# Performance work log

Hardware: AMD Instinct MI355X
Metric: run time of the kernel (lower is better)

The kernel has to match this reference:

```python
import jax, jax.numpy as jnp
from jax import lax
import numpy as np

B, CIN, COUT, D, TDIM, E = 2, 16, 8, 96, 256, 8


def setup_inputs() -> dict:
    key = jax.random.key(0)
    ks = jax.random.split(key, 12)
    s = lambda fan: 1.0 / np.sqrt(fan)
    return {
        "x": jax.random.normal(ks[0], (B, CIN, D, D, D), jnp.float32),
        "text_features": jax.random.normal(ks[1], (B, TDIM), jnp.float32),
        # expert weight basis [E, Cout, Cin, 3, 3, 3] (kaiming-uniform-ish)
        "weight_basis": jax.random.uniform(ks[2], (E, COUT, CIN, 3, 3, 3), jnp.float32, -s(CIN * 27), s(CIN * 27)),
        "bias_basis": jnp.zeros((E, COUT), jnp.float32),
        # router MLP: text_dim -> 64 -> E
        "r_w1": jax.random.uniform(ks[3], (TDIM, 64), jnp.float32, -s(TDIM), s(TDIM)),
        "r_b1": jax.random.uniform(ks[4], (64,), jnp.float32, -s(TDIM), s(TDIM)),
        "r_w2": jax.random.uniform(ks[5], (64, E), jnp.float32, -s(64), s(64)),
        "r_b2": jax.random.uniform(ks[6], (E,), jnp.float32, -s(64), s(64)),
        # modulator MLP: text_dim -> 64 -> Cout
        "m_w1": jax.random.uniform(ks[7], (TDIM, 64), jnp.float32, -s(TDIM), s(TDIM)),
        "m_b1": jax.random.uniform(ks[8], (64,), jnp.float32, -s(TDIM), s(TDIM)),
        "m_w2": jax.random.uniform(ks[9], (64, COUT), jnp.float32, -s(64), s(64)),
        "m_b2": jax.random.uniform(ks[10], (COUT,), jnp.float32, -s(64), s(64)),
    }


def reference(x, text_features, weight_basis, bias_basis,
              r_w1, r_b1, r_w2, r_b2, m_w1, m_b1, m_w2, m_b2):
    b, cin = x.shape[0], x.shape[1]
    cout = weight_basis.shape[1]
    # router -> softmax routing weights over experts
    h = jax.nn.leaky_relu(text_features @ r_w1 + r_b1, 0.1)
    router_logits = h @ r_w2 + r_b2                      # [b, E]
    routing_weights = jax.nn.softmax(router_logits, -1)  # [b, E]
    # modulator -> per-sample channel gates
    g = jax.nn.leaky_relu(text_features @ m_w1 + m_b1, 0.1)
    gamma = jax.nn.sigmoid(g @ m_w2 + m_b2)              # [b, Cout]
    # per-sample dynamic conv weights via expert mixing
    cw = jnp.einsum('be,eoixyz->boixyz', routing_weights, weight_basis)  # [b,Cout,Cin,3,3,3]
    cb = routing_weights @ bias_basis                                    # [b, Cout]
    # grouped-conv trick: batch folded into channels, groups=b
    xr = x.reshape(1, b * cin, *x.shape[2:])
    wr = cw.reshape(b * cout, cin, 3, 3, 3)
    out = lax.conv_general_dilated(
        xr, wr, window_strides=(1, 1, 1), padding=[(1, 1)] * 3,
        dimension_numbers=('NCDHW', 'OIDHW', 'NCDHW'), feature_group_count=b)
    out = out.reshape(b, cout, *out.shape[2:]) + cb[:, :, None, None, None]
    out = out * (1.0 + gamma[:, :, None, None, None])
    return out, router_logits, routing_weights
```

## Files before the change

### kernel.cpp

```cpp
#include <hip/hip_runtime.h>
#include <math.h>

#define NB 2
#define CIN 16
#define COUT 8
#define DD 96
#define TDIM 256
#define NE 8
#define VOX (DD*DD*DD)
#define OUT_ELEMS (NB*COUT*VOX)

#define XT_BYTES ((size_t)NB * VOX * 32)
#define WS_A_F 7168
#define WS_D_F 7184

#define LX 18
#define PLANE (LX*LX)
#define NVX (PLANE*5)
#define HALFB (NVX*16)

typedef _Float16 f16x8 __attribute__((ext_vector_type(8)));
typedef _Float16 f16x4 __attribute__((ext_vector_type(4)));
typedef float f32x4 __attribute__((ext_vector_type(4)));

__global__ void setup_kernel(const float* __restrict__ text,
                             const float* __restrict__ wb,
                             const float* __restrict__ bb,
                             const float* __restrict__ rw1, const float* __restrict__ rb1,
                             const float* __restrict__ rw2, const float* __restrict__ rb2,
                             const float* __restrict__ mw1, const float* __restrict__ mb1,
                             const float* __restrict__ mw2, const float* __restrict__ mb2,
                             float* __restrict__ dout_tail,
                             char* __restrict__ tab)
{
    __shared__ float h[NB][64], g[NB][64], logits[NB][NE], rw[NB][NE];
    const int t = threadIdx.x;
    float* tabf = (float*)tab;

    if (t < 128) {
        const int b = t >> 6, j = t & 63;
        float acc = rb1[j];
        for (int k = 0; k < TDIM; ++k) acc = fmaf(text[b*TDIM + k], rw1[k*64 + j], acc);
        h[b][j] = (acc >= 0.f) ? acc : 0.1f * acc;
    } else {
        const int tt = t - 128, b = tt >> 6, j = tt & 63;
        float acc = mb1[j];
        for (int k = 0; k < TDIM; ++k) acc = fmaf(text[b*TDIM + k], mw1[k*64 + j], acc);
        g[b][j] = (acc >= 0.f) ? acc : 0.1f * acc;
    }
    __syncthreads();

    if (t < NB*NE) {
        const int b = t >> 3, e = t & 7;
        float acc = rb2[e];
        for (int k = 0; k < 64; ++k) acc = fmaf(h[b][k], rw2[k*NE + e], acc);
        logits[b][e] = acc;
        dout_tail[t] = acc;
    }
    __syncthreads();

    if (t < NB*NE) {
        const int b = t >> 3, e = t & 7;
        float mx = logits[b][0];
        for (int k = 1; k < NE; ++k) mx = fmaxf(mx, logits[b][k]);
        float s = 0.f;
        for (int k = 0; k < NE; ++k) s += expf(logits[b][k] - mx);
        const float w = expf(logits[b][e] - mx) / s;
        rw[b][e] = w;
        dout_tail[NB*NE + t] = w;
    }
    __syncthreads();

    if (t < NB*COUT) {
        const int b = t >> 3, co = t & 7;
        float acc = mb2[co];
        for (int k = 0; k < 64; ++k) acc = fmaf(g[b][k], mw2[k*COUT + co], acc);
        const float gamma = 1.f / (1.f + expf(-acc));
        const float a = 1.f + gamma;
        float cb = 0.f;
        for (int e = 0; e < NE; ++e) cb = fmaf(rw[b][e], bb[e*COUT + co], cb);
        tabf[WS_A_F + t] = a;
        tabf[WS_D_F + t] = cb * a;
    }

    for (int idx = t; idx < 2*14*64*8; idx += 256) {
        const int b  = (idx >= 7168) ? 1 : 0;
        const int r  = idx - b*7168;
        const int c  = r >> 9;
        const int l  = (r >> 3) & 63;
        const int j  = idx & 7;
        const int q  = l >> 4;
        const int n  = l & 15;
        const int p  = q & 1;
        const int ci = (q >> 1)*8 + j;
        int tap;
        if (c < 9)        tap = (c/3)*9 + (c%3)*3 + p;
        else if (c < 12)  tap = (c-9)*9 + p*3 + 2;
        else if (c == 12) tap = p*9 + 8;
        else              tap = p ? -1 : 26;
        float v = 0.f;
        if (n < 8 && tap >= 0) {
            for (int e = 0; e < NE; ++e)
                v = fmaf(rw[b][e], wb[((e*COUT + n)*CIN + ci)*27 + tap], v);
        }
        ((_Float16*)tab)[idx] = (_Float16)v;
    }
}

#define TV 1024
__global__ __launch_bounds__(256) void transpose_kernel(
    const float* __restrict__ x, _Float16* __restrict__ xt)
{
    __shared__ _Float16 buf[CIN][TV];
    const int t  = threadIdx.x;
    const int b  = blockIdx.y;
    const int v0 = blockIdx.x * TV;
    const float* __restrict__ xb = x + (size_t)b * CIN * VOX + v0;

    #pragma unroll
    for (int ci = 0; ci < CIN; ++ci) {
        const float4 f = ((const float4*)(xb + (size_t)ci * VOX))[t];
        f16x4 hv;
        hv[0] = (_Float16)f.x; hv[1] = (_Float16)f.y;
        hv[2] = (_Float16)f.z; hv[3] = (_Float16)f.w;
        *(f16x4*)&buf[ci][t*4] = hv;
    }
    __syncthreads();

    #pragma unroll
    for (int i = 0; i < TV/256; ++i) {
        const int v = i*256 + t;
        union { _Float16 h[16]; uint4 u[2]; } o;
        #pragma unroll
        for (int ci = 0; ci < CIN; ++ci) o.h[ci] = buf[ci][v];
        uint4* __restrict__ dst = (uint4*)(xt + (size_t)(b*VOX + v0 + v) * 16);
        dst[0] = o.u[0];
        dst[1] = o.u[1];
    }
}

__global__ __launch_bounds__(256) void conv_mfma(
    const _Float16* __restrict__ xt,
    const char* __restrict__ tab,
    float* __restrict__ out)
{
    __shared__ char lds[2*HALFB];
    const int tid  = threadIdx.x;
    const int lane = tid & 63;
    const int wv   = tid >> 6;
    const int b    = blockIdx.z;
    const int z0   = blockIdx.y * 3;
    const int xti  = blockIdx.x % 6;
    const int yti  = blockIdx.x / 6;
    const int x0   = xti * 16, y0 = yti * 16;

    const f16x8* __restrict__ bfp = (const f16x8*)tab;
    f16x8 bfrag[14];
    #pragma unroll
    for (int c = 0; c < 14; ++c)
        bfrag[c] = bfp[(b*14 + c)*64 + lane];

    const _Float16* __restrict__ xtb = xt + (size_t)b * VOX * 16;
    for (int s = tid; s < NVX; s += 256) {
        const int lz = s / PLANE;
        const int r1 = s - lz * PLANE;
        const int ly = r1 / LX;
        const int lx = r1 - ly * LX;
        const int zg = z0 - 1 + lz, yg = y0 - 1 + ly, xg = x0 - 1 + lx;
        const bool ok = ((unsigned)zg < 96u) & ((unsigned)yg < 96u) & ((unsigned)xg < 96u);
        const int zc = ok ? zg : 0, yc = ok ? yg : 0, xc = ok ? xg : 0;
        const uint4* __restrict__ p = (const uint4*)(xtb + (size_t)((zc*DD + yc)*DD + xc) * 16);
        uint4 lo = {0,0,0,0}, hi = {0,0,0,0};
        if (ok) { lo = p[0]; hi = p[1]; }
        *(uint4*)&lds[s*16]         = lo;
        *(uint4*)&lds[HALFB + s*16] = hi;
    }
    __syncthreads();

    const int q    = lane >> 4;
    const int m    = lane & 15;
    const int pbit = q & 1;
    const int hbit = q >> 1;

    const float* tabf = (const float*)tab;
    const float a_n = tabf[WS_A_F + b*8 + (m & 7)];
    const float d_n = tabf[WS_D_F + b*8 + (m & 7)];

    constexpr int OFFB[14] = {0,288,576,5184,5472,5760,10368,10656,10944,
                              32,5216,10400,608,10976};

    const int com = hbit*HALFB + m*16;
    const int dA = pbit*16, dB = pbit*288, dC = pbit*5184;

    #pragma unroll
    for (int t = 0; t < 12; ++t) {
        const int zi = t >> 2;
        const int yi = wv*4 + (t & 3);
        const char* __restrict__ base = &lds[(zi*PLANE + yi*LX)*16 + com];

        f16x8 af[14];
        #pragma unroll
        for (int c = 0; c < 9; ++c)  af[c] = *(const f16x8*)(base + dA + OFFB[c]);
        #pragma unroll
        for (int c = 9; c < 12; ++c) af[c] = *(const f16x8*)(base + dB + OFFB[c]);
        af[12] = *(const f16x8*)(base + dC + OFFB[12]);
        af[13] = *(const f16x8*)(base + OFFB[13]);

        f32x4 acc0 = {0.f,0.f,0.f,0.f}, acc1 = {0.f,0.f,0.f,0.f};
        #pragma unroll
        for (int c = 0; c < 14; c += 2) {
            acc0 = __builtin_amdgcn_mfma_f32_16x16x32_f16(af[c],   bfrag[c],   acc0, 0, 0, 0);
            acc1 = __builtin_amdgcn_mfma_f32_16x16x32_f16(af[c+1], bfrag[c+1], acc1, 0, 0, 0);
        }

        if (m < 8) {
            const int zz = z0 + zi, yy = y0 + yi;
            float* __restrict__ op = out + (size_t)(b*COUT + m)*VOX
                                        + (size_t)(zz*DD + yy)*DD + x0 + q*4;
            f32x4 res;
            #pragma unroll
            for (int r = 0; r < 4; ++r) res[r] = fmaf(acc0[r] + acc1[r], a_n, d_n);
            *reinterpret_cast<f32x4*>(op) = res;
        }
    }
}

extern "C" void kernel_launch(void* const* d_in, const int* in_sizes, int n_in,
                              void* d_out, int out_size, void* d_ws, size_t ws_size,
                              hipStream_t stream) {
    const float* x    = (const float*)d_in[0];
    const float* text = (const float*)d_in[1];
    const float* wb   = (const float*)d_in[2];
    const float* bb   = (const float*)d_in[3];
    const float* rw1  = (const float*)d_in[4];
    const float* rb1  = (const float*)d_in[5];
    const float* rw2  = (const float*)d_in[6];
    const float* rb2  = (const float*)d_in[7];
    const float* mw1  = (const float*)d_in[8];
    const float* mb1  = (const float*)d_in[9];
    const float* mw2  = (const float*)d_in[10];
    const float* mb2  = (const float*)d_in[11];

    float* out = (float*)d_out;
    _Float16* xt = (_Float16*)d_ws;
    char* tab = (char*)d_ws + XT_BYTES;

    setup_kernel<<<1, 256, 0, stream>>>(text, wb, bb, rw1, rb1, rw2, rb2,
                                        mw1, mb1, mw2, mb2,
                                        out + OUT_ELEMS, tab);

    transpose_kernel<<<dim3(VOX/TV, NB), 256, 0, stream>>>(x, xt);

    conv_mfma<<<dim3(36, 32, NB), 256, 0, stream>>>(xt, tab, out);
}
```

Measured before the change: 290.0 us.

## Fuse setup into transpose kernel and reuse z-plane A fragments across loop

The single-block setup kernel is folded into the transpose launch as one extra block per batch sample, which removes one kernel launch and lets setup run alongside the transpose. The conv loop is reorganised from a flat 12-iteration loop into a y-outer, z-inner loop that keeps a sliding window of A/G fragments in registers, so each z step loads only the new plane from LDS. This reduces LDS reads per tile at the cost of more live registers, which could lower occupancy.

```diff
diff --git a/kernel.cpp b/kernel.cpp
--- a/kernel.cpp
+++ b/kernel.cpp
@@ -19,101 +19,90 @@
 #define NVX (PLANE*5)
 #define HALFB (NVX*16)
 
+#define TV 1024
+#define NTB (VOX/TV)
+
 typedef _Float16 f16x8 __attribute__((ext_vector_type(8)));
 typedef _Float16 f16x4 __attribute__((ext_vector_type(4)));
 typedef float f32x4 __attribute__((ext_vector_type(4)));
 
-__global__ void setup_kernel(const float* __restrict__ text,
-                             const float* __restrict__ wb,
-                             const float* __restrict__ bb,
-                             const float* __restrict__ rw1, const float* __restrict__ rb1,
-                             const float* __restrict__ rw2, const float* __restrict__ rb2,
-                             const float* __restrict__ mw1, const float* __restrict__ mb1,
-                             const float* __restrict__ mw2, const float* __restrict__ mb2,
-                             float* __restrict__ dout_tail,
-                             char* __restrict__ tab)
-{
-    __shared__ float h[NB][64], g[NB][64], logits[NB][NE], rw[NB][NE];
-    const int t = threadIdx.x;
-    float* tabf = (float*)tab;
-
-    if (t < 128) {
-        const int b = t >> 6, j = t & 63;
-        float acc = rb1[j];
-        for (int k = 0; k < TDIM; ++k) acc = fmaf(text[b*TDIM + k], rw1[k*64 + j], acc);
-        h[b][j] = (acc >= 0.f) ? acc : 0.1f * acc;
-    } else {
-        const int tt = t - 128, b = tt >> 6, j = tt & 63;
-        float acc = mb1[j];
-        for (int k = 0; k < TDIM; ++k) acc = fmaf(text[b*TDIM + k], mw1[k*64 + j], acc);
-        g[b][j] = (acc >= 0.f) ? acc : 0.1f * acc;
-    }
-    __syncthreads();
-
-    if (t < NB*NE) {
-        const int b = t >> 3, e = t & 7;
-        float acc = rb2[e];
-        for (int k = 0; k < 64; ++k) acc = fmaf(h[b][k], rw2[k*NE + e], acc);
-        logits[b][e] = acc;
-        dout_tail[t] = acc;
-    }
-    __syncthreads();
-
-    if (t < NB*NE) {
-        const int b = t >> 3, e = t & 7;
-        float mx = logits[b][0];
-        for (int k = 1; k < NE; ++k) mx = fmaxf(mx, logits[b][k]);
-        float s = 0.f;
-        for (int k = 0; k < NE; ++k) s += expf(logits[b][k] - mx);
-        const float w = expf(logits[b][e] - mx) / s;
-        rw[b][e] = w;
-        dout_tail[NB*NE + t] = w;
-    }
-    __syncthreads();
-
-    if (t < NB*COUT) {
-        const int b = t >> 3, co = t & 7;
-        float acc = mb2[co];
-        for (int k = 0; k < 64; ++k) acc = fmaf(g[b][k], mw2[k*COUT + co], acc);
-        const float gamma = 1.f / (1.f + expf(-acc));
-        const float a = 1.f + gamma;
-        float cb = 0.f;
-        for (int e = 0; e < NE; ++e) cb = fmaf(rw[b][e], bb[e*COUT + co], cb);
-        tabf[WS_A_F + t] = a;
-        tabf[WS_D_F + t] = cb * a;
-    }
-
-    for (int idx = t; idx < 2*14*64*8; idx += 256) {
-        const int b  = (idx >= 7168) ? 1 : 0;
-        const int r  = idx - b*7168;
-        const int c  = r >> 9;
-        const int l  = (r >> 3) & 63;
-        const int j  = idx & 7;
-        const int q  = l >> 4;
-        const int n  = l & 15;
-        const int p  = q & 1;
-        const int ci = (q >> 1)*8 + j;
-        int tap;
-        if (c < 9)        tap = (c/3)*9 + (c%3)*3 + p;
-        else if (c < 12)  tap = (c-9)*9 + p*3 + 2;
-        else if (c == 12) tap = p*9 + 8;
-        else              tap = p ? -1 : 26;
-        float v = 0.f;
-        if (n < 8 && tap >= 0) {
-            for (int e = 0; e < NE; ++e)
-                v = fmaf(rw[b][e], wb[((e*COUT + n)*CIN + ci)*27 + tap], v);
-        }
-        ((_Float16*)tab)[idx] = (_Float16)v;
-    }
-}
-
-#define TV 1024
-__global__ __launch_bounds__(256) void transpose_kernel(
-    const float* __restrict__ x, _Float16* __restrict__ xt)
+__global__ __launch_bounds__(256) void transpose_setup(
+    const float* __restrict__ x, _Float16* __restrict__ xt,
+    const float* __restrict__ text,
+    const float* __restrict__ wb,
+    const float* __restrict__ bb,
+    const float* __restrict__ rw1, const float* __restrict__ rb1,
+    const float* __restrict__ rw2, const float* __restrict__ rb2,
+    const float* __restrict__ mw1, const float* __restrict__ mb1,
+    const float* __restrict__ mw2, const float* __restrict__ mb2,
+    float* __restrict__ dout_tail,
+    char* __restrict__ tab)
 {
     __shared__ _Float16 buf[CIN][TV];
-    const int t  = threadIdx.x;
-    const int b  = blockIdx.y;
+    __shared__ float hg[2][64], logits[NE], rwv[NE];
+    const int t = threadIdx.x;
+    const int b = blockIdx.y;
+
+    if (blockIdx.x == NTB) {
+        if (t < 128) {
+            const int which = t >> 6, j = t & 63;
+            const float* w1 = which ? mw1 : rw1;
+            const float* b1 = which ? mb1 : rb1;
+            float acc = b1[j];
+            for (int k = 0; k < TDIM; ++k) acc = fmaf(text[b*TDIM + k], w1[k*64 + j], acc);
+            hg[which][j] = (acc >= 0.f) ? acc : 0.1f * acc;
+        }
+        __syncthreads();
+        if (t < NE) {
+            float acc = rb2[t];
+            for (int k = 0; k < 64; ++k) acc = fmaf(hg[0][k], rw2[k*NE + t], acc);
+            logits[t] = acc;
+            dout_tail[b*NE + t] = acc;
+        }
+        __syncthreads();
+        if (t < NE) {
+            float mx = logits[0];
+            for (int k = 1; k < NE; ++k) mx = fmaxf(mx, logits[k]);
+            float s = 0.f;
+            for (int k = 0; k < NE; ++k) s += expf(logits[k] - mx);
+            const float w = expf(logits[t] - mx) / s;
+            rwv[t] = w;
+            dout_tail[NB*NE + b*NE + t] = w;
+        }
+        __syncthreads();
+        if (t < COUT) {
+            float acc = mb2[t];
+            for (int k = 0; k < 64; ++k) acc = fmaf(hg[1][k], mw2[k*COUT + t], acc);
+            const float gamma = 1.f / (1.f + expf(-acc));
+            const float a = 1.f + gamma;
+            float cb = 0.f;
+            for (int e = 0; e < NE; ++e) cb = fmaf(rwv[e], bb[e*COUT + t], cb);
+            ((float*)tab)[WS_A_F + b*COUT + t] = a;
+            ((float*)tab)[WS_D_F + b*COUT + t] = cb * a;
+        }
+        for (int r = t; r < 14*64*8; r += 256) {
+            const int c  = r >> 9;
+            const int l  = (r >> 3) & 63;
+            const int j  = r & 7;
+            const int q  = l >> 4;
+            const int n  = l & 15;
+            const int p  = q & 1;
+            const int ci = (q >> 1)*8 + j;
+            int tap;
+            if (c < 9)        tap = (c/3)*9 + (c%3)*3 + p;
+            else if (c < 12)  tap = (c-9)*9 + p*3 + 2;
+            else if (c == 12) tap = p*9 + 8;
+            else              tap = p ? -1 : 26;
+            float v = 0.f;
+            if (n < 8 && tap >= 0) {
+                for (int e = 0; e < NE; ++e)
+                    v = fmaf(rwv[e], wb[((e*COUT + n)*CIN + ci)*27 + tap], v);
+            }
+            ((_Float16*)tab)[b*7168 + r] = (_Float16)v;
+        }
+        return;
+    }
+
     const int v0 = blockIdx.x * TV;
     const float* __restrict__ xb = x + (size_t)b * CIN * VOX + v0;
 
@@ -186,43 +175,68 @@
     const float a_n = tabf[WS_A_F + b*8 + (m & 7)];
     const float d_n = tabf[WS_D_F + b*8 + (m & 7)];
 
-    constexpr int OFFB[14] = {0,288,576,5184,5472,5760,10368,10656,10944,
-                              32,5216,10400,608,10976};
-
     const int com = hbit*HALFB + m*16;
-    const int dA = pbit*16, dB = pbit*288, dC = pbit*5184;
-
-    #pragma unroll
-    for (int t = 0; t < 12; ++t) {
-        const int zi = t >> 2;
-        const int yi = wv*4 + (t & 3);
-        const char* __restrict__ base = &lds[(zi*PLANE + yi*LX)*16 + com];
-
-        f16x8 af[14];
+    const int dA = pbit*16;
+    const int dB = pbit*288;
+    const int dC = pbit*5184;
+
+    #define LD_A(p_, dy_)  (*(const f16x8*)&lds[((p_)*PLANE + (yi+(dy_))*LX)*16 + com + dA])
+    #define LD_G(p_)       (*(const f16x8*)&lds[((p_)*PLANE + yi*LX + 2)*16 + com + dB])
+    #define LD_H12(zi_)    (*(const f16x8*)&lds[((zi_)*PLANE + (yi+2)*LX + 2)*16 + com + dC])
+    #define LD_H13(zi_)    (*(const f16x8*)&lds[(((zi_)+2)*PLANE + (yi+2)*LX + 2)*16 + com])
+
+    #pragma unroll
+    for (int yi4 = 0; yi4 < 4; ++yi4) {
+        const int yi = wv*4 + yi4;
+
+        f16x8 A[3][3], G[3];
         #pragma unroll
-        for (int c = 0; c < 9; ++c)  af[c] = *(const f16x8*)(base + dA + OFFB[c]);
+        for (int dy = 0; dy < 3; ++dy) { A[0][dy] = LD_A(0, dy); A[1][dy] = LD_A(1, dy); }
+        G[0] = LD_G(0); G[1] = LD_G(1);
+
         #pragma unroll
-        for (int c = 9; c < 12; ++c) af[c] = *(const f16x8*)(base + dB + OFFB[c]);
-        af[12] = *(const f16x8*)(base + dC + OFFB[12]);
-        af[13] = *(const f16x8*)(base + OFFB[13]);
-
-        f32x4 acc0 = {0.f,0.f,0.f,0.f}, acc1 = {0.f,0.f,0.f,0.f};
-        #pragma unroll
-        for (int c = 0; c < 14; c += 2) {
-            acc0 = __builtin_amdgcn_mfma_f32_16x16x32_f16(af[c],   bfrag[c],   acc0, 0, 0, 0);
-            acc1 = __builtin_amdgcn_mfma_f32_16x16x32_f16(af[c+1], bfrag[c+1], acc1, 0, 0, 0);
-        }
-
-        if (m < 8) {
-            const int zz = z0 + zi, yy = y0 + yi;
-            float* __restrict__ op = out + (size_t)(b*COUT + m)*VOX
-                                        + (size_t)(zz*DD + yy)*DD + x0 + q*4;
-            f32x4 res;
+        for (int zi = 0; zi < 3; ++zi) {
             #pragma unroll
-            for (int r = 0; r < 4; ++r) res[r] = fmaf(acc0[r] + acc1[r], a_n, d_n);
-            *reinterpret_cast<f32x4*>(op) = res;
-        }
-    }
+            for (int dy = 0; dy < 3; ++dy) A[2][dy] = LD_A(zi+2, dy);
+            G[2] = LD_G(zi+2);
+            const f16x8 H12v = LD_H12(zi);
+            const f16x8 H13v = LD_H13(zi);
+
+            f32x4 acc0 = {0.f,0.f,0.f,0.f}, acc1 = {0.f,0.f,0.f,0.f};
+            acc0 = __builtin_amdgcn_mfma_f32_16x16x32_f16(A[0][0], bfrag[0],  acc0, 0,0,0);
+            acc1 = __builtin_amdgcn_mfma_f32_16x16x32_f16(A[0][1], bfrag[1],  acc1, 0,0,0);
+            acc0 = __builtin_amdgcn_mfma_f32_16x16x32_f16(A[0][2], bfrag[2],  acc0, 0,0,0);
+            acc1 = __builtin_amdgcn_mfma_f32_16x16x32_f16(A[1][0], bfrag[3],  acc1, 0,0,0);
+            acc0 = __builtin_amdgcn_mfma_f32_16x16x32_f16(A[1][1], bfrag[4],  acc0, 0,0,0);
+            acc1 = __builtin_amdgcn_mfma_f32_16x16x32_f16(A[1][2], bfrag[5],  acc1, 0,0,0);
+            acc0 = __builtin_amdgcn_mfma_f32_16x16x32_f16(A[2][0], bfrag[6],  acc0, 0,0,0);
+            acc1 = __builtin_amdgcn_mfma_f32_16x16x32_f16(A[2][1], bfrag[7],  acc1, 0,0,0);
+            acc0 = __builtin_amdgcn_mfma_f32_16x16x32_f16(A[2][2], bfrag[8],  acc0, 0,0,0);
+            acc1 = __builtin_amdgcn_mfma_f32_16x16x32_f16(G[0],    bfrag[9],  acc1, 0,0,0);
+            acc0 = __builtin_amdgcn_mfma_f32_16x16x32_f16(G[1],    bfrag[10], acc0, 0,0,0);
+            acc1 = __builtin_amdgcn_mfma_f32_16x16x32_f16(G[2],    bfrag[11], acc1, 0,0,0);
+            acc0 = __builtin_amdgcn_mfma_f32_16x16x32_f16(H12v,    bfrag[12], acc0, 0,0,0);
+            acc1 = __builtin_amdgcn_mfma_f32_16x16x32_f16(H13v,    bfrag[13], acc1, 0,0,0);
+
+            if (m < 8) {
+                const int zz = z0 + zi, yy = y0 + yi;
+                float* __restrict__ op = out + (size_t)(b*COUT + m)*VOX
+                                            + (size_t)(zz*DD + yy)*DD + x0 + q*4;
+                f32x4 res;
+                #pragma unroll
+                for (int r = 0; r < 4; ++r) res[r] = fmaf(acc0[r] + acc1[r], a_n, d_n);
+                *reinterpret_cast<f32x4*>(op) = res;
+            }
+
+            #pragma unroll
+            for (int dy = 0; dy < 3; ++dy) { A[0][dy] = A[1][dy]; A[1][dy] = A[2][dy]; }
+            G[0] = G[1]; G[1] = G[2];
+        }
+    }
+    #undef LD_A
+    #undef LD_G
+    #undef LD_H12
+    #undef LD_H13
 }
 
 extern "C" void kernel_launch(void* const* d_in, const int* in_sizes, int n_in,
@@ -245,11 +259,9 @@
     _Float16* xt = (_Float16*)d_ws;
     char* tab = (char*)d_ws + XT_BYTES;
 
-    setup_kernel<<<1, 256, 0, stream>>>(text, wb, bb, rw1, rb1, rw2, rb2,
-                                        mw1, mb1, mw2, mb2,
-                                        out + OUT_ELEMS, tab);
-
-    transpose_kernel<<<dim3(VOX/TV, NB), 256, 0, stream>>>(x, xt);
+    transpose_setup<<<dim3(NTB + 1, NB), 256, 0, stream>>>(
+        x, xt, text, wb, bb, rw1, rb1, rw2, rb2, mw1, mb1, mw2, mb2,
+        out + OUT_ELEMS, tab);
 
     conv_mfma<<<dim3(36, 32, NB), 256, 0, stream>>>(xt, tab, out);
 }
```

Result: faster. 266.2 us (-8.2%).
